# Kernel optimization log

Measured on AMD Instinct MI355X. Metric: run time of the kernel, lower is better.

## Reference

```python
import jax, jax.numpy as jnp
import numpy as np

NUM_HEADS = 16
INPUT_DIM = 1024  # == dim == qkv_scale


def setup_inputs() -> dict:
    key = jax.random.key(0)
    k1, k2, k3 = jax.random.split(key, 3)
    x = jax.random.normal(k1, (4, 2048, INPUT_DIM), dtype=jnp.float32)
    # torch Linear(input_dim, 3*dim): y = x @ W.T + b; we store W pre-transposed as [in, out]
    W_qkv = jax.random.normal(k2, (INPUT_DIM, 3 * INPUT_DIM), dtype=jnp.float32) * (INPUT_DIM ** -0.5)
    b_qkv = jax.random.normal(k3, (3 * INPUT_DIM,), dtype=jnp.float32) * 0.01
    return {"x": x, "W_qkv": W_qkv, "b_qkv": b_qkv}


def reference(x, W_qkv, b_qkv):
    b, n, _ = x.shape
    h = NUM_HEADS
    d = INPUT_DIM // h
    scale = INPUT_DIM ** 0.5  # qkv_scale**0.5, MULTIPLIED (no softmax, no division)

    qkv = x @ W_qkv + b_qkv                      # [b, n, 3*dim]
    # rearrange 'b n (h d k) -> k b h n d': last axis splits (h, d, 3), k fastest
    qkv = qkv.reshape(b, n, h, d, 3)
    q = jnp.transpose(qkv[..., 0], (0, 2, 1, 3))  # [b, h, n, d]
    k_ = jnp.transpose(qkv[..., 1], (0, 2, 1, 3))
    v = jnp.transpose(qkv[..., 2], (0, 2, 1, 3))

    attn = jnp.einsum('bhid,bhjd->bhij', q, k_) * scale  # [b, h, n, n]
    out = jnp.einsum('bhij,bhjd->bhid', attn, v)         # [b, h, n, d]
    return out
```

## Files before the change

kernel.cpp:

```cpp
#include <hip/hip_runtime.h>
#include <stdint.h>

#define DEV __device__ __forceinline__

typedef float f32x4 __attribute__((ext_vector_type(4)));
typedef __bf16 bf16x8 __attribute__((ext_vector_type(8)));
typedef short short8 __attribute__((ext_vector_type(8)));
typedef short short4v __attribute__((ext_vector_type(4)));

DEV unsigned short f2bf(float f) {
    union { float f; unsigned u; } c; c.f = f;
    unsigned u = c.u;
    u += 0x7fffu + ((u >> 16) & 1u);
    return (unsigned short)(u >> 16);
}
DEV void async_ld16(const void* g, void* l) {
    __builtin_amdgcn_global_load_lds(
        (const __attribute__((address_space(1))) unsigned int*)g,
        (__attribute__((address_space(3))) unsigned int*)l, 16, 0, 0);
}
DEV f32x4 mfma16(bf16x8 a, bf16x8 b, f32x4 c) {
    return __builtin_amdgcn_mfma_f32_16x16x32_bf16(a, b, c, 0, 0, 0);
}

__global__ __launch_bounds__(256) void k_prep(const float* __restrict__ x,
                                              const float* __restrict__ W,
                                              unsigned short* __restrict__ xb,
                                              unsigned short* __restrict__ Wt) {
    __shared__ float T[64][65];
    const int blk = blockIdx.x, t = threadIdx.x;
    if (blk < 4096) {
        int i = blk * 256 + t;
        const float4* xp = (const float4*)x;
        float4 a = xp[i * 2], b = xp[i * 2 + 1];
        short8 o;
        o[0] = (short)f2bf(a.x); o[1] = (short)f2bf(a.y);
        o[2] = (short)f2bf(a.z); o[3] = (short)f2bf(a.w);
        o[4] = (short)f2bf(b.x); o[5] = (short)f2bf(b.y);
        o[6] = (short)f2bf(b.z); o[7] = (short)f2bf(b.w);
        *(short8*)(xb + i * 8) = o;
    } else {
        int bx = blk - 4096;
        int k0 = (bx / 48) * 64, n0 = (bx % 48) * 64;
        int rr = t >> 4, c4 = (t & 15) * 4;
        for (int i = 0; i < 4; i++) {
            int row = rr + i * 16;
            float4 v = *(const float4*)(W + (unsigned)(k0 + row) * 3072u + n0 + c4);
            T[row][c4] = v.x; T[row][c4 + 1] = v.y; T[row][c4 + 2] = v.z; T[row][c4 + 3] = v.w;
        }
        __syncthreads();
        for (int i = 0; i < 4; i++) {
            int ncol = rr + i * 16;
            int n = n0 + ncol;
            int which = n % 3;
            int oc = (n / 192) * 64 + (n % 192) / 3;
            short4v o;
            o[0] = (short)f2bf(T[c4 + 0][ncol]);
            o[1] = (short)f2bf(T[c4 + 1][ncol]);
            o[2] = (short)f2bf(T[c4 + 2][ncol]);
            o[3] = (short)f2bf(T[c4 + 3][ncol]);
            *(short4v*)(Wt + (unsigned)which * 1048576u + (unsigned)oc * 1024u + k0 + c4) = o;
        }
    }
}

#define BARRIER() asm volatile("s_barrier" ::: "memory")
#define WAITV(n) do { asm volatile("s_waitcnt vmcnt(" #n ")" ::: "memory"); \
                      __builtin_amdgcn_sched_barrier(0); } while (0)

__global__ __launch_bounds__(512, 2) void k_qkv(const unsigned short* __restrict__ xb,
                                                const unsigned short* __restrict__ Wt,
                                                const float* __restrict__ bias,
                                                unsigned short* __restrict__ Qs,
                                                unsigned short* __restrict__ K,
                                                unsigned short* __restrict__ V) {
    __shared__ __align__(16) unsigned short As[2][256 * 64];
    __shared__ __align__(16) unsigned short Bs[2][256 * 64];

    const int o = blockIdx.x;
    const int w = (o & 7) * 48 + (o >> 3);
    const int mtile = w & 31, ntile = w >> 5;
    const int m0 = mtile * 256;
    const int plane = ntile >> 2;
    const int pc0 = (ntile & 3) * 256;
    const unsigned short* Xp = xb + (unsigned)m0 * 1024u;
    const unsigned short* Wp = Wt + (unsigned)plane * 1048576u + (unsigned)pc0 * 1024u;

    const int t = threadIdx.x;
    const int wave = t >> 6, lane = t & 63;
    const int lan15 = lane & 15, quad = lane >> 4;
    const int slr = t >> 3;
    const int scs = t & 7;

    const bool swp = (plane == 0);
    const int aRow0 = (wave & 1) * 128;
    const int bRow0 = (wave >> 1) * 64;

    f32x4 acc[8][4] = {};

#define STAGE(kt, bf) do {                                                    \
        const unsigned ko_ = (unsigned)((kt) * 64);                           \
        _Pragma("unroll")                                                     \
        for (int i_ = 0; i_ < 4; i_++) {                                      \
            int r_ = i_ * 64 + slr;                                           \
            int c_ = scs ^ (r_ & 7);                                          \
            async_ld16(Xp + (unsigned)r_ * 1024u + ko_ + c_ * 8,              \
                       (void*)(As[bf] + (i_ * 64 + wave * 8) * 64));          \
            async_ld16(Wp + (unsigned)r_ * 1024u + ko_ + c_ * 8,              \
                       (void*)(Bs[bf] + (i_ * 64 + wave * 8) * 64));          \
        }                                                                     \
    } while (0)

    STAGE(0, 0);

    for (int kt = 0; kt < 16; kt++) {
        const int buf = kt & 1;
        if (kt < 15) { STAGE(kt + 1, buf ^ 1); WAITV(8); }
        else         { WAITV(0); }
        BARRIER();

        const unsigned short* Aop = swp ? Bs[buf] : As[buf];
        const unsigned short* Bop = swp ? As[buf] : Bs[buf];
#pragma unroll
        for (int ks = 0; ks < 2; ks++) {
            const int c0 = ks * 4 + quad;
            bf16x8 af[8], bfr[4];
#pragma unroll
            for (int tn = 0; tn < 4; tn++) {
                int row = bRow0 + tn * 16 + lan15;
                bfr[tn] = *(const bf16x8*)(Bop + row * 64 + (c0 ^ (row & 7)) * 8);
            }
#pragma unroll
            for (int tm = 0; tm < 8; tm++) {
                int row = aRow0 + tm * 16 + lan15;
                af[tm] = *(const bf16x8*)(Aop + row * 64 + (c0 ^ (row & 7)) * 8);
            }
            __builtin_amdgcn_s_setprio(1);
#pragma unroll
            for (int tm = 0; tm < 8; tm++)
#pragma unroll
                for (int tn = 0; tn < 4; tn++)
                    acc[tm][tn] = mfma16(af[tm], bfr[tn], acc[tm][tn]);
            __builtin_amdgcn_s_setprio(0);
        }
        BARRIER();
    }
#undef STAGE

    if (plane == 0) {
        const int cg = (wave & 1) * 128;
        const int tg = (wave >> 1) * 64;
#pragma unroll
        for (int tm = 0; tm < 8; tm++) {
            int c4 = pc0 + cg + tm * 16 + quad * 4;
            int h = c4 >> 6, dd = c4 & 63;
            float b0 = bias[h * 192 + (dd + 0) * 3];
            float b1 = bias[h * 192 + (dd + 1) * 3];
            float b2 = bias[h * 192 + (dd + 2) * 3];
            float b3 = bias[h * 192 + (dd + 3) * 3];
#pragma unroll
            for (int tn = 0; tn < 4; tn++) {
                int token = m0 + tg + tn * 16 + lan15;
                unsigned bb = (unsigned)(token >> 11), tl = (unsigned)(token & 2047);
                uint2 p;
                p.x = (unsigned)f2bf((acc[tm][tn][0] + b0) * 32.0f) |
                      ((unsigned)f2bf((acc[tm][tn][1] + b1) * 32.0f) << 16);
                p.y = (unsigned)f2bf((acc[tm][tn][2] + b2) * 32.0f) |
                      ((unsigned)f2bf((acc[tm][tn][3] + b3) * 32.0f) << 16);
                *(uint2*)(Qs + bb * 2097152u + tl * 1024u + c4) = p;
            }
        }
    } else {
        unsigned short* dst = (plane == 1) ? K : V;
        const int tg = (wave & 1) * 128;
        const int cg = (wave >> 1) * 64;
        const int batch = m0 >> 11;
#pragma unroll
        for (int tn = 0; tn < 4; tn++) {
            int cip = pc0 + cg + tn * 16 + lan15;
            int h = cip >> 6, d = cip & 63;
            float bv = bias[h * 192 + d * 3 + plane];
            unsigned kv_base = ((unsigned)(batch * 16 + h) * 64u + (unsigned)d) * 2048u;
#pragma unroll
            for (int tm = 0; tm < 8; tm++) {
                unsigned token0 = (unsigned)((m0 + tg + tm * 16 + quad * 4) & 2047);
                uint2 p;
                p.x = (unsigned)f2bf(acc[tm][tn][0] + bv) |
                      ((unsigned)f2bf(acc[tm][tn][1] + bv) << 16);
                p.y = (unsigned)f2bf(acc[tm][tn][2] + bv) |
                      ((unsigned)f2bf(acc[tm][tn][3] + bv) << 16);
                *(uint2*)(dst + kv_base + token0) = p;
            }
        }
    }
}

__global__ __launch_bounds__(256) void k_attn4(const unsigned short* __restrict__ Kt,
                                               const unsigned short* __restrict__ Vt,
                                               const unsigned short* __restrict__ Qs,
                                               float* __restrict__ out) {
    __shared__ __align__(16) unsigned short Ks[64 * 128];
    __shared__ __align__(16) unsigned short Vs[64 * 128];
    __shared__ __align__(16) unsigned short Msb[64 * 64];
    const int bh = blockIdx.x & 63, sub = blockIdx.x >> 6;
    const int b = bh >> 4, h = bh & 15;
    const int wave = threadIdx.x >> 6, lane = threadIdx.x & 63;
    const int lan15 = lane & 15, quad = lane >> 4;
    const unsigned base = (unsigned)bh * 131072u;
    const int mt0 = (wave & 1) * 2, nt0 = (wave >> 1) * 2;
    const int slr = wave * 16 + (lane >> 4), scs = lane & 15;

    f32x4 macc[2][2] = {};
    for (int j = 0; j < 16; j++) {
        __syncthreads();
        for (int i = 0; i < 4; i++) {
            int lr = slr + i * 4;
            int c = scs ^ (lr & 15);
            async_ld16(Kt + base + (unsigned)lr * 2048u + j * 128 + c * 8,
                       (void*)(Ks + (wave * 16 + i * 4) * 128));
            async_ld16(Vt + base + (unsigned)lr * 2048u + j * 128 + c * 8,
                       (void*)(Vs + (wave * 16 + i * 4) * 128));
        }
        __syncthreads();
        for (int ks2 = 0; ks2 < 4; ks2++) {
            int c0 = ks2 * 4 + quad;
            bf16x8 ak[2], bv[2];
            for (int i = 0; i < 2; i++) {
                int row = (mt0 + i) * 16 + lan15;
                ak[i] = *(const bf16x8*)(Ks + row * 128 + (c0 ^ (row & 15)) * 8);
            }
            for (int i = 0; i < 2; i++) {
                int row = (nt0 + i) * 16 + lan15;
                bv[i] = *(const bf16x8*)(Vs + row * 128 + (c0 ^ (row & 15)) * 8);
            }
            for (int i = 0; i < 2; i++)
                for (int j2 = 0; j2 < 2; j2++)
                    macc[i][j2] = mfma16(ak[i], bv[j2], macc[i][j2]);
        }
    }
    for (int i = 0; i < 2; i++)
        for (int j2 = 0; j2 < 2; j2++) {
            int d2 = (nt0 + j2) * 16 + lan15;
            int c4 = ((mt0 + i) * 4 + quad) ^ (d2 & 15);
            uint2 p;
            p.x = (unsigned)f2bf(macc[i][j2][0]) | ((unsigned)f2bf(macc[i][j2][1]) << 16);
            p.y = (unsigned)f2bf(macc[i][j2][2]) | ((unsigned)f2bf(macc[i][j2][3]) << 16);
            *(uint2*)(Msb + d2 * 64 + c4 * 4) = p;
        }
    __syncthreads();

    const int t0 = sub * 256 + wave * 64;
    f32x4 oacc[4][4] = {};
#pragma unroll
    for (int ks = 0; ks < 2; ks++) {
        bf16x8 af[4], bfr[4];
        for (int mt = 0; mt < 4; mt++) {
            int tok = t0 + mt * 16 + lan15;
            af[mt] = *(const bf16x8*)(Qs + (unsigned)b * 2097152u + (unsigned)tok * 1024u +
                                      h * 64 + ks * 32 + quad * 8);
        }
        for (int nt = 0; nt < 4; nt++) {
            int d2 = nt * 16 + lan15;
            int cA = ks * 8 + quad * 2;
            uint2 u0 = *(const uint2*)(Msb + d2 * 64 + ((cA) ^ (d2 & 15)) * 4);
            uint2 u1 = *(const uint2*)(Msb + d2 * 64 + ((cA + 1) ^ (d2 & 15)) * 4);
            union { uint4 u; bf16x8 v; } cv;
            cv.u.x = u0.x; cv.u.y = u0.y; cv.u.z = u1.x; cv.u.w = u1.y;
            bfr[nt] = cv.v;
        }
        for (int mt = 0; mt < 4; mt++)
            for (int nt = 0; nt < 4; nt++)
                oacc[mt][nt] = mfma16(af[mt], bfr[nt], oacc[mt][nt]);
    }
    for (int mt = 0; mt < 4; mt++)
        for (int nt = 0; nt < 4; nt++)
            for (int r = 0; r < 4; r++)
                out[base + (unsigned)(t0 + mt * 16 + quad * 4 + r) * 64u + nt * 16 + lan15] =
                    oacc[mt][nt][r];
}

extern "C" void kernel_launch(void* const* d_in, const int* in_sizes, int n_in,
                              void* d_out, int out_size, void* d_ws, size_t ws_size,
                              hipStream_t stream) {
    const float* x = (const float*)d_in[0];
    const float* W = (const float*)d_in[1];
    const float* b = (const float*)d_in[2];
    float* out = (float*)d_out;

    unsigned short* xb = (unsigned short*)d_ws;
    unsigned short* Wt = xb + 8388608;
    unsigned short* Qs = Wt + 3145728;
    unsigned short* Kt = Qs + 8388608;
    unsigned short* Vt = Kt + 8388608;

    k_prep<<<4864, 256, 0, stream>>>(x, W, xb, Wt);
    k_qkv<<<384, 512, 0, stream>>>(xb, Wt, b, Qs, Kt, Vt);
    k_attn4<<<512, 256, 0, stream>>>(Kt, Vt, Qs, out);
}
```

Measured before the change: 191.9 us.

## Quarter-phase pipeline QKV GEMM, split K^T V reduction into separate kernels

The QKV GEMM main loop is split into four quadrant phases. Each phase issues the next k-tile's half-tile loads just before computing one 128x128 quadrant, so loads overlap with MFMA work at a finer grain. The attention kernel, which recomputed the full K^T V product in every one of its 512 blocks, is split in two. A 256-block kernel computes four partial K^T V chunks per head into fp32 scratch, and a second kernel sums the partials and applies them to Q with vectorized float4 output stores. This removes the 8x redundant K^T V work at the cost of an extra launch, scratch traffic, and more barriers per k-step.

```diff
diff --git a/kernel.cpp b/kernel.cpp
--- a/kernel.cpp
+++ b/kernel.cpp
@@ -78,8 +78,8 @@
     __shared__ __align__(16) unsigned short Bs[2][256 * 64];
 
     const int o = blockIdx.x;
-    const int w = (o & 7) * 48 + (o >> 3);
-    const int mtile = w & 31, ntile = w >> 5;
+    const int w_ = (o & 7) * 48 + (o >> 3);
+    const int mtile = w_ & 31, ntile = w_ >> 5;
     const int m0 = mtile * 256;
     const int plane = ntile >> 2;
     const int pc0 = (ntile & 3) * 256;
@@ -93,117 +93,151 @@
     const int scs = t & 7;
 
     const bool swp = (plane == 0);
-    const int aRow0 = (wave & 1) * 128;
-    const int bRow0 = (wave >> 1) * 64;
-
-    f32x4 acc[8][4] = {};
-
-#define STAGE(kt, bf) do {                                                    \
-        const unsigned ko_ = (unsigned)((kt) * 64);                           \
+    const int am = (wave & 1) * 64;
+    const int bn = (wave >> 1) * 32;
+
+    f32x4 acc[2][2][4][2] = {};
+
+#define STAGE_A(kt1, h, bf) do {                                              \
+        const unsigned ko_ = (unsigned)((kt1) * 64);                          \
         _Pragma("unroll")                                                     \
-        for (int i_ = 0; i_ < 4; i_++) {                                      \
-            int r_ = i_ * 64 + slr;                                           \
+        for (int i_ = 0; i_ < 2; i_++) {                                      \
+            int r_ = (h) * 128 + i_ * 64 + slr;                               \
             int c_ = scs ^ (r_ & 7);                                          \
             async_ld16(Xp + (unsigned)r_ * 1024u + ko_ + c_ * 8,              \
-                       (void*)(As[bf] + (i_ * 64 + wave * 8) * 64));          \
-            async_ld16(Wp + (unsigned)r_ * 1024u + ko_ + c_ * 8,              \
-                       (void*)(Bs[bf] + (i_ * 64 + wave * 8) * 64));          \
+                       (void*)(As[bf] + ((h) * 128 + i_ * 64 + wave * 8) * 64)); \
         }                                                                     \
     } while (0)
-
-    STAGE(0, 0);
+#define STAGE_B(kt1, h, bf) do {                                              \
+        const unsigned ko_ = (unsigned)((kt1) * 64);                          \
+        _Pragma("unroll")                                                     \
+        for (int i_ = 0; i_ < 2; i_++) {                                      \
+            int r_ = (h) * 128 + i_ * 64 + slr;                               \
+            int c_ = scs ^ (r_ & 7);                                          \
+            async_ld16(Wp + (unsigned)r_ * 1024u + ko_ + c_ * 8,              \
+                       (void*)(Bs[bf] + ((h) * 128 + i_ * 64 + wave * 8) * 64)); \
+        }                                                                     \
+    } while (0)
+
+#define PHASE_COMPUTE(bf, ah, bh) do {                                        \
+        const unsigned short* Aop = swp ? Bs[bf] : As[bf];                    \
+        const unsigned short* Bop = swp ? As[bf] : Bs[bf];                    \
+        bf16x8 af[2][4], bfr[2][2];                                           \
+        _Pragma("unroll")                                                     \
+        for (int ks = 0; ks < 2; ks++) {                                      \
+            const int c0 = ks * 4 + quad;                                     \
+            _Pragma("unroll")                                                 \
+            for (int tm = 0; tm < 4; tm++) {                                  \
+                int row = (ah) * 128 + am + tm * 16 + lan15;                  \
+                af[ks][tm] = *(const bf16x8*)(Aop + row * 64 +                \
+                                              (c0 ^ (row & 7)) * 8);          \
+            }                                                                 \
+            _Pragma("unroll")                                                 \
+            for (int tn = 0; tn < 2; tn++) {                                  \
+                int row = (bh) * 128 + bn + tn * 16 + lan15;                  \
+                bfr[ks][tn] = *(const bf16x8*)(Bop + row * 64 +               \
+                                               (c0 ^ (row & 7)) * 8);         \
+            }                                                                 \
+        }                                                                     \
+        __builtin_amdgcn_s_setprio(1);                                        \
+        _Pragma("unroll")                                                     \
+        for (int ks = 0; ks < 2; ks++)                                        \
+            _Pragma("unroll")                                                 \
+            for (int tm = 0; tm < 4; tm++)                                    \
+                _Pragma("unroll")                                             \
+                for (int tn = 0; tn < 2; tn++)                                \
+                    acc[ah][bh][tm][tn] =                                     \
+                        mfma16(af[ks][tm], bfr[ks][tn], acc[ah][bh][tm][tn]); \
+        __builtin_amdgcn_s_setprio(0);                                        \
+    } while (0)
+
+    STAGE_A(0, 0, 0);
+    STAGE_B(0, 0, 0);
+    STAGE_B(0, 1, 0);
+    STAGE_A(0, 1, 0);
 
     for (int kt = 0; kt < 16; kt++) {
-        const int buf = kt & 1;
-        if (kt < 15) { STAGE(kt + 1, buf ^ 1); WAITV(8); }
-        else         { WAITV(0); }
+        const int bf = kt & 1, nb = bf ^ 1;
+        const bool pf = (kt < 15);
+        WAITV(4);
         BARRIER();
-
-        const unsigned short* Aop = swp ? Bs[buf] : As[buf];
-        const unsigned short* Bop = swp ? As[buf] : Bs[buf];
-#pragma unroll
-        for (int ks = 0; ks < 2; ks++) {
-            const int c0 = ks * 4 + quad;
-            bf16x8 af[8], bfr[4];
-#pragma unroll
-            for (int tn = 0; tn < 4; tn++) {
-                int row = bRow0 + tn * 16 + lan15;
-                bfr[tn] = *(const bf16x8*)(Bop + row * 64 + (c0 ^ (row & 7)) * 8);
-            }
-#pragma unroll
-            for (int tm = 0; tm < 8; tm++) {
-                int row = aRow0 + tm * 16 + lan15;
-                af[tm] = *(const bf16x8*)(Aop + row * 64 + (c0 ^ (row & 7)) * 8);
-            }
-            __builtin_amdgcn_s_setprio(1);
-#pragma unroll
-            for (int tm = 0; tm < 8; tm++)
-#pragma unroll
-                for (int tn = 0; tn < 4; tn++)
-                    acc[tm][tn] = mfma16(af[tm], bfr[tn], acc[tm][tn]);
-            __builtin_amdgcn_s_setprio(0);
-        }
+        if (pf) STAGE_A(kt + 1, 0, nb);
+        PHASE_COMPUTE(bf, 0, 0);
+        if (pf) { WAITV(4); } else { WAITV(2); }
         BARRIER();
-    }
-#undef STAGE
+        if (pf) STAGE_B(kt + 1, 0, nb);
+        PHASE_COMPUTE(bf, 0, 1);
+        if (pf) { WAITV(4); } else { WAITV(0); }
+        BARRIER();
+        if (pf) STAGE_B(kt + 1, 1, nb);
+        PHASE_COMPUTE(bf, 1, 1);
+        BARRIER();
+        if (pf) STAGE_A(kt + 1, 1, nb);
+        PHASE_COMPUTE(bf, 1, 0);
+    }
+#undef STAGE_A
+#undef STAGE_B
+#undef PHASE_COMPUTE
 
     if (plane == 0) {
-        const int cg = (wave & 1) * 128;
-        const int tg = (wave >> 1) * 64;
-#pragma unroll
-        for (int tm = 0; tm < 8; tm++) {
-            int c4 = pc0 + cg + tm * 16 + quad * 4;
-            int h = c4 >> 6, dd = c4 & 63;
-            float b0 = bias[h * 192 + (dd + 0) * 3];
-            float b1 = bias[h * 192 + (dd + 1) * 3];
-            float b2 = bias[h * 192 + (dd + 2) * 3];
-            float b3 = bias[h * 192 + (dd + 3) * 3];
-#pragma unroll
-            for (int tn = 0; tn < 4; tn++) {
-                int token = m0 + tg + tn * 16 + lan15;
-                unsigned bb = (unsigned)(token >> 11), tl = (unsigned)(token & 2047);
-                uint2 p;
-                p.x = (unsigned)f2bf((acc[tm][tn][0] + b0) * 32.0f) |
-                      ((unsigned)f2bf((acc[tm][tn][1] + b1) * 32.0f) << 16);
-                p.y = (unsigned)f2bf((acc[tm][tn][2] + b2) * 32.0f) |
-                      ((unsigned)f2bf((acc[tm][tn][3] + b3) * 32.0f) << 16);
-                *(uint2*)(Qs + bb * 2097152u + tl * 1024u + c4) = p;
-            }
-        }
+#pragma unroll
+        for (int ah = 0; ah < 2; ah++)
+#pragma unroll
+            for (int tm = 0; tm < 4; tm++) {
+                int c4 = pc0 + ah * 128 + am + tm * 16 + quad * 4;
+                int h = c4 >> 6, dd = c4 & 63;
+                float b0 = bias[h * 192 + (dd + 0) * 3];
+                float b1 = bias[h * 192 + (dd + 1) * 3];
+                float b2 = bias[h * 192 + (dd + 2) * 3];
+                float b3 = bias[h * 192 + (dd + 3) * 3];
+#pragma unroll
+                for (int bh = 0; bh < 2; bh++)
+#pragma unroll
+                    for (int tn = 0; tn < 2; tn++) {
+                        int token = m0 + bh * 128 + bn + tn * 16 + lan15;
+                        unsigned bb = (unsigned)(token >> 11), tl = (unsigned)(token & 2047);
+                        f32x4 a = acc[ah][bh][tm][tn];
+                        uint2 p;
+                        p.x = (unsigned)f2bf((a[0] + b0) * 32.0f) |
+                              ((unsigned)f2bf((a[1] + b1) * 32.0f) << 16);
+                        p.y = (unsigned)f2bf((a[2] + b2) * 32.0f) |
+                              ((unsigned)f2bf((a[3] + b3) * 32.0f) << 16);
+                        *(uint2*)(Qs + bb * 2097152u + tl * 1024u + c4) = p;
+                    }
+            }
     } else {
         unsigned short* dst = (plane == 1) ? K : V;
-        const int tg = (wave & 1) * 128;
-        const int cg = (wave >> 1) * 64;
         const int batch = m0 >> 11;
 #pragma unroll
-        for (int tn = 0; tn < 4; tn++) {
-            int cip = pc0 + cg + tn * 16 + lan15;
-            int h = cip >> 6, d = cip & 63;
-            float bv = bias[h * 192 + d * 3 + plane];
-            unsigned kv_base = ((unsigned)(batch * 16 + h) * 64u + (unsigned)d) * 2048u;
-#pragma unroll
-            for (int tm = 0; tm < 8; tm++) {
-                unsigned token0 = (unsigned)((m0 + tg + tm * 16 + quad * 4) & 2047);
-                uint2 p;
-                p.x = (unsigned)f2bf(acc[tm][tn][0] + bv) |
-                      ((unsigned)f2bf(acc[tm][tn][1] + bv) << 16);
-                p.y = (unsigned)f2bf(acc[tm][tn][2] + bv) |
-                      ((unsigned)f2bf(acc[tm][tn][3] + bv) << 16);
-                *(uint2*)(dst + kv_base + token0) = p;
-            }
-        }
-    }
-}
-
-__global__ __launch_bounds__(256) void k_attn4(const unsigned short* __restrict__ Kt,
-                                               const unsigned short* __restrict__ Vt,
-                                               const unsigned short* __restrict__ Qs,
-                                               float* __restrict__ out) {
+        for (int bh = 0; bh < 2; bh++)
+#pragma unroll
+            for (int tn = 0; tn < 2; tn++) {
+                int cip = pc0 + bh * 128 + bn + tn * 16 + lan15;
+                int h = cip >> 6, d = cip & 63;
+                float bv = bias[h * 192 + d * 3 + plane];
+                unsigned kv_base = ((unsigned)(batch * 16 + h) * 64u + (unsigned)d) * 2048u;
+#pragma unroll
+                for (int ah = 0; ah < 2; ah++)
+#pragma unroll
+                    for (int tm = 0; tm < 4; tm++) {
+                        unsigned token0 =
+                            (unsigned)((m0 + ah * 128 + am + tm * 16 + quad * 4) & 2047);
+                        f32x4 a = acc[ah][bh][tm][tn];
+                        uint2 p;
+                        p.x = (unsigned)f2bf(a[0] + bv) | ((unsigned)f2bf(a[1] + bv) << 16);
+                        p.y = (unsigned)f2bf(a[2] + bv) | ((unsigned)f2bf(a[3] + bv) << 16);
+                        *(uint2*)(dst + kv_base + token0) = p;
+                    }
+            }
+    }
+}
+
+__global__ __launch_bounds__(256) void k_m(const unsigned short* __restrict__ Kt,
+                                           const unsigned short* __restrict__ Vt,
+                                           float* __restrict__ Mp) {
     __shared__ __align__(16) unsigned short Ks[64 * 128];
     __shared__ __align__(16) unsigned short Vs[64 * 128];
-    __shared__ __align__(16) unsigned short Msb[64 * 64];
-    const int bh = blockIdx.x & 63, sub = blockIdx.x >> 6;
-    const int b = bh >> 4, h = bh & 15;
+    const int bh = blockIdx.x & 63, chunk = blockIdx.x >> 6;
     const int wave = threadIdx.x >> 6, lane = threadIdx.x & 63;
     const int lan15 = lane & 15, quad = lane >> 4;
     const unsigned base = (unsigned)bh * 131072u;
@@ -211,7 +245,7 @@
     const int slr = wave * 16 + (lane >> 4), scs = lane & 15;
 
     f32x4 macc[2][2] = {};
-    for (int j = 0; j < 16; j++) {
+    for (int j = chunk * 4; j < chunk * 4 + 4; j++) {
         __syncthreads();
         for (int i = 0; i < 4; i++) {
             int lr = slr + i * 4;
@@ -241,42 +275,72 @@
     for (int i = 0; i < 2; i++)
         for (int j2 = 0; j2 < 2; j2++) {
             int d2 = (nt0 + j2) * 16 + lan15;
-            int c4 = ((mt0 + i) * 4 + quad) ^ (d2 & 15);
+            int d1b = (mt0 + i) * 16 + quad * 4;
+            *(f32x4*)(Mp + (((unsigned)(bh * 4 + chunk) * 64u + (unsigned)d2) * 64u + d1b)) =
+                macc[i][j2];
+        }
+}
+
+__global__ __launch_bounds__(256) void k_out(const float* __restrict__ Mp,
+                                             const unsigned short* __restrict__ Qs,
+                                             float* __restrict__ out) {
+    __shared__ __align__(16) unsigned short Msb[64 * 64];
+    const int bh = blockIdx.x & 63, sub = blockIdx.x >> 6;
+    const int b = bh >> 4, h = bh & 15;
+    const int wave = threadIdx.x >> 6, lane = threadIdx.x & 63;
+    const int lan15 = lane & 15, quad = lane >> 4;
+    const unsigned base = (unsigned)bh * 131072u;
+
+    {
+        const int t = threadIdx.x;
+        const int d2 = t >> 2, d1b = (t & 3) * 16;
+        const float* mp0 = Mp + (((unsigned)(bh * 4) * 64u + (unsigned)d2) * 64u + d1b);
+#pragma unroll
+        for (int jj = 0; jj < 4; jj++) {
+            float4 s = *(const float4*)(mp0 + jj * 4);
+#pragma unroll
+            for (int c = 1; c < 4; c++) {
+                float4 v = *(const float4*)(mp0 + (unsigned)c * 4096u + jj * 4);
+                s.x += v.x; s.y += v.y; s.z += v.z; s.w += v.w;
+            }
+            int c4 = (t & 3) * 4 + jj;
             uint2 p;
-            p.x = (unsigned)f2bf(macc[i][j2][0]) | ((unsigned)f2bf(macc[i][j2][1]) << 16);
-            p.y = (unsigned)f2bf(macc[i][j2][2]) | ((unsigned)f2bf(macc[i][j2][3]) << 16);
-            *(uint2*)(Msb + d2 * 64 + c4 * 4) = p;
-        }
+            p.x = (unsigned)f2bf(s.x) | ((unsigned)f2bf(s.y) << 16);
+            p.y = (unsigned)f2bf(s.z) | ((unsigned)f2bf(s.w) << 16);
+            *(uint2*)(Msb + d2 * 64 + (c4 ^ (d2 & 15)) * 4) = p;
+        }
+    }
     __syncthreads();
 
     const int t0 = sub * 256 + wave * 64;
     f32x4 oacc[4][4] = {};
 #pragma unroll
     for (int ks = 0; ks < 2; ks++) {
-        bf16x8 af[4], bfr[4];
-        for (int mt = 0; mt < 4; mt++) {
-            int tok = t0 + mt * 16 + lan15;
-            af[mt] = *(const bf16x8*)(Qs + (unsigned)b * 2097152u + (unsigned)tok * 1024u +
-                                      h * 64 + ks * 32 + quad * 8);
-        }
-        for (int nt = 0; nt < 4; nt++) {
-            int d2 = nt * 16 + lan15;
+        bf16x8 mf[4], qf[4];
+        for (int tm = 0; tm < 4; tm++) {
+            int d2 = tm * 16 + lan15;
             int cA = ks * 8 + quad * 2;
             uint2 u0 = *(const uint2*)(Msb + d2 * 64 + ((cA) ^ (d2 & 15)) * 4);
             uint2 u1 = *(const uint2*)(Msb + d2 * 64 + ((cA + 1) ^ (d2 & 15)) * 4);
             union { uint4 u; bf16x8 v; } cv;
             cv.u.x = u0.x; cv.u.y = u0.y; cv.u.z = u1.x; cv.u.w = u1.y;
-            bfr[nt] = cv.v;
-        }
-        for (int mt = 0; mt < 4; mt++)
-            for (int nt = 0; nt < 4; nt++)
-                oacc[mt][nt] = mfma16(af[mt], bfr[nt], oacc[mt][nt]);
-    }
-    for (int mt = 0; mt < 4; mt++)
-        for (int nt = 0; nt < 4; nt++)
-            for (int r = 0; r < 4; r++)
-                out[base + (unsigned)(t0 + mt * 16 + quad * 4 + r) * 64u + nt * 16 + lan15] =
-                    oacc[mt][nt][r];
+            mf[tm] = cv.v;
+        }
+        for (int tn = 0; tn < 4; tn++) {
+            int tok = t0 + tn * 16 + lan15;
+            qf[tn] = *(const bf16x8*)(Qs + (unsigned)b * 2097152u + (unsigned)tok * 1024u +
+                                      h * 64 + ks * 32 + quad * 8);
+        }
+        for (int tm = 0; tm < 4; tm++)
+            for (int tn = 0; tn < 4; tn++)
+                oacc[tm][tn] = mfma16(mf[tm], qf[tn], oacc[tm][tn]);
+    }
+    for (int tm = 0; tm < 4; tm++)
+        for (int tn = 0; tn < 4; tn++) {
+            int tok = t0 + tn * 16 + lan15;
+            int d2b = tm * 16 + quad * 4;
+            *(f32x4*)(out + base + (unsigned)tok * 64u + d2b) = oacc[tm][tn];
+        }
 }
 
 extern "C" void kernel_launch(void* const* d_in, const int* in_sizes, int n_in,
@@ -292,8 +356,10 @@
     unsigned short* Qs = Wt + 3145728;
     unsigned short* Kt = Qs + 8388608;
     unsigned short* Vt = Kt + 8388608;
+    float* Mp = (float*)xb;
 
     k_prep<<<4864, 256, 0, stream>>>(x, W, xb, Wt);
     k_qkv<<<384, 512, 0, stream>>>(xb, Wt, b, Qs, Kt, Vt);
-    k_attn4<<<512, 256, 0, stream>>>(Kt, Vt, Qs, out);
-}
+    k_m<<<256, 256, 0, stream>>>(Kt, Vt, Mp);
+    k_out<<<512, 256, 0, stream>>>(Mp, Qs, out);
+}
```

After: 225.0 us. +17.2%, slower.
